# Performance work log

Measured on AMD Instinct MI355X. Metric: run time of the kernel, lower is better.

## Reference

```python
import jax, jax.numpy as jnp
import numpy as np

B, S, H, D = 1, 2048, 24, 128   # batch, img seq, heads, head_dim
RD = 64                          # rotary_emb_dim (partial RoPE)
IPS, IPD = 512, 1152             # ip tokens, ip feature dim
HID = H * D                      # 3072
EPS = 1e-6


def _heads(x):
    # (B, S, H*D) -> (B, H, S, D)
    b, s, _ = x.shape
    return x.reshape(b, s, H, D).transpose(0, 2, 1, 3)


def _rmsnorm(x, scale):
    # RMSNorm with p<0 path: rms = ||x||_2 / sqrt(D); y = scale * x / (rms + eps)
    rms = jnp.linalg.norm(x, axis=-1, keepdims=True) * (D ** -0.5)
    return scale * (x / (rms + EPS))


def _rope(x, sin, cos):
    # rotate-half RoPE on first RD channels, pass-through on the rest
    xr, xp = x[..., :RD], x[..., RD:]
    x1, x2 = jnp.split(xr, 2, axis=-1)
    rot = jnp.concatenate([-x2, x1], axis=-1)
    return jnp.concatenate([xr * cos + rot * sin, xp], axis=-1)


def setup_inputs() -> dict:
    key = jax.random.key(0)
    ks = jax.random.split(key, 16)
    std = 0.02
    inp = {
        "hidden_states": jax.random.normal(ks[0], (B, S, HID), jnp.float32),
        "ip_hidden_states": jax.random.normal(ks[1], (B, IPS, IPD), jnp.float32),
        "sin": jax.random.normal(ks[2], (S, RD), jnp.float32),
        "cos": jax.random.normal(ks[3], (S, RD), jnp.float32),
        "Wq": jax.random.normal(ks[4], (HID, HID), jnp.float32) * std,
        "bq": jnp.zeros((HID,), jnp.float32),
        "Wk": jax.random.normal(ks[5], (HID, HID), jnp.float32) * std,
        "bk": jnp.zeros((HID,), jnp.float32),
        "Wv": jax.random.normal(ks[6], (HID, HID), jnp.float32) * std,
        "bv": jnp.zeros((HID,), jnp.float32),
        "Wo": jax.random.normal(ks[7], (HID, HID), jnp.float32) * std,
        "bo": jnp.zeros((HID,), jnp.float32),
        "Wk_ip": jax.random.normal(ks[8], (HID, IPD), jnp.float32) * std,
        "bk_ip": jnp.zeros((HID,), jnp.float32),
        "Wv_ip": jax.random.normal(ks[9], (HID, IPD), jnp.float32) * std,
        "bv_ip": jnp.zeros((HID,), jnp.float32),
        "q_scale": jnp.ones((D,), jnp.float32),
        "k_scale": jnp.ones((D,), jnp.float32),
    }
    return inp


def reference(hidden_states, ip_hidden_states, sin, cos,
              Wq, bq, Wk, bk, Wv, bv, Wo, bo,
              Wk_ip, bk_ip, Wv_ip, bv_ip, q_scale, k_scale):
    scale = 1.0  # default `scale` kwarg
    # projections (self-attention: encoder_hidden_states = hidden_states)
    q = _heads(hidden_states @ Wq.T + bq)        # (B,H,S,D)
    k = _heads(hidden_states @ Wk.T + bk)
    v = _heads(hidden_states @ Wv.T + bv)
    k_ip = _heads(ip_hidden_states @ Wk_ip.T + bk_ip)   # (B,H,IPS,D)
    v_ip = _heads(ip_hidden_states @ Wv_ip.T + bv_ip)

    # IP branch uses RMS-normed, head_dim^-0.5-scaled, UNROTATED q and k_ip
    # (key_ip is rotated in the source but the rotated value is never used)
    q_norm = _rmsnorm(q, q_scale) * (D ** -0.5)
    k_ip_norm = _rmsnorm(k_ip, k_scale) * (D ** -0.5)

    # main branch: RoPE'd q/k, raw dot product (alpha=1.0, no 1/sqrt(d))
    q_rot = _rope(q, sin, cos)
    k_rot = _rope(k, sin, cos)

    scores = jnp.einsum('bhsd,bhtd->bhst', q_rot, k_rot)
    probs = jax.nn.softmax(scores, axis=-1)
    scores_ip = scale * jnp.einsum('bhsd,bhtd->bhst', q_norm, k_ip_norm)
    probs_ip = jax.nn.softmax(scores_ip, axis=-1)

    out = jnp.einsum('bhst,bhtd->bhsd', probs, v) \
        + jnp.einsum('bhst,bhtd->bhsd', probs_ip, v_ip)
    out = out.transpose(0, 2, 1, 3).reshape(B, S, HID)  # batch_to_head_dim
    out = out @ Wo.T + bo                                # to_out[0]; dropout = id
    return out
```

## Files before the change

### kernel.cpp

```cpp
#include <hip/hip_runtime.h>
#include <stdint.h>

#define S_LEN 2048
#define NH    24
#define HD    128
#define HID   3072
#define IPS   512
#define IPD   1152

using f16   = __fp16;
using f16x4 = __fp16 __attribute__((ext_vector_type(4)));
using f16x8 = __fp16 __attribute__((ext_vector_type(8)));
using f32x4 = float  __attribute__((ext_vector_type(4)));

__device__ __forceinline__ void glds16(const f16* g, f16* l) {
  __builtin_amdgcn_global_load_lds((const __attribute__((address_space(1))) void*)g,
                                   (__attribute__((address_space(3))) void*)l,
                                   16, 0, 0);
}

__global__ void k_cvt(const float* __restrict__ src, f16* __restrict__ dst, int n4) {
  int i = blockIdx.x * 256 + threadIdx.x;
  if (i >= n4) return;
  float4 v = ((const float4*)src)[i];
  f16x4 o;
  o.x = (f16)v.x; o.y = (f16)v.y; o.z = (f16)v.z; o.w = (f16)v.w;
  ((f16x4*)dst)[i] = o;
}

__global__ __launch_bounds__(256) void k_gemm_nt(
    const f16* __restrict__ A,
    const f16* __restrict__ B0, const f16* __restrict__ B1, const f16* __restrict__ B2,
    const float* __restrict__ bias0, const float* __restrict__ bias1, const float* __restrict__ bias2,
    void* __restrict__ C0, void* __restrict__ C1, void* __restrict__ C2,
    int M, int N, int K, int out_f32)
{
  const int z = blockIdx.z;
  const f16*   B    = (z == 0) ? B0 : (z == 1) ? B1 : B2;
  const float* bias = (z == 0) ? bias0 : (z == 1) ? bias1 : bias2;
  void*        Cv   = (z == 0) ? C0 : (z == 1) ? C1 : C2;

  __shared__ f16 As[128 * 32];
  __shared__ f16 Bs[128 * 32];

  const int tid  = threadIdx.x;
  const int w    = tid >> 6, l = tid & 63;
  const int quad = l >> 4,  l16 = l & 15;
  const int bm = blockIdx.y * 128, bn = blockIdx.x * 128;
  const int wm = (w >> 1) * 64,    wn = (w & 1) * 64;

  f32x4 acc[4][4] = {};

  const int r0 = w * 32;
  const f16* Ag = A + (bm + r0 + (l >> 2)) * K + (l & 3) * 8;
  const f16* Bg = B + (bn + r0 + (l >> 2)) * K + (l & 3) * 8;
  f16* lA0 = &As[r0 * 32];
  f16* lA1 = &As[(r0 + 16) * 32];
  f16* lB0 = &Bs[r0 * 32];
  f16* lB1 = &Bs[(r0 + 16) * 32];
  const int kstride16 = 16 * K;

  for (int k0 = 0; k0 < K; k0 += 32) {
    glds16(Ag + k0,             lA0);
    glds16(Ag + kstride16 + k0, lA1);
    glds16(Bg + k0,             lB0);
    glds16(Bg + kstride16 + k0, lB1);
    __syncthreads();

    f16x8 af[4], bf[4];
#pragma unroll
    for (int i = 0; i < 4; i++)
      af[i] = *(const f16x8*)&As[(wm + i * 16 + l16) * 32 + quad * 8];
#pragma unroll
    for (int j = 0; j < 4; j++)
      bf[j] = *(const f16x8*)&Bs[(wn + j * 16 + l16) * 32 + quad * 8];
#pragma unroll
    for (int i = 0; i < 4; i++)
#pragma unroll
      for (int j = 0; j < 4; j++)
        acc[i][j] = __builtin_amdgcn_mfma_f32_16x16x32_f16(af[i], bf[j], acc[i][j], 0, 0, 0);
    __syncthreads();
  }

  float bv[4];
#pragma unroll
  for (int j = 0; j < 4; j++) bv[j] = bias[bn + wn + j * 16 + l16];

#pragma unroll
  for (int i = 0; i < 4; i++) {
    const int row0 = bm + wm + i * 16 + quad * 4;
#pragma unroll
    for (int j = 0; j < 4; j++) {
      const int col = bn + wn + j * 16 + l16;
#pragma unroll
      for (int r = 0; r < 4; r++) {
        float v = acc[i][j][r] + bv[j];
        if (out_f32) ((float*)Cv)[(row0 + r) * N + col] = v;
        else         ((f16*)Cv)[(row0 + r) * N + col] = (f16)v;
      }
    }
  }
}

__global__ void k_rope(const f16* __restrict__ x, const float* __restrict__ snp,
                       const float* __restrict__ csp, f16* __restrict__ out, int total) {
  int idx = blockIdx.x * 256 + threadIdx.x;
  if (idx >= total) return;
  int s = idx / HID;
  int c = idx - s * HID;
  int d = c & (HD - 1);
  float v = (float)x[idx];
  float r;
  if (d < 64) {
    float cs = csp[s * 64 + d], sn = snp[s * 64 + d];
    if (d < 32) r = v * cs - (float)x[idx + 32] * sn;
    else        r = v * cs + (float)x[idx - 32] * sn;
  } else {
    r = v;
  }
  out[idx] = (f16)r;
}

__global__ void k_rmsnorm(const f16* __restrict__ x, const float* __restrict__ scale,
                          f16* __restrict__ out, int rows) {
  int gw = (blockIdx.x * 256 + threadIdx.x) >> 6;
  int l  = threadIdx.x & 63;
  if (gw >= rows) return;
  int base = gw * HD;
  float a = (float)x[base + 2 * l];
  float b = (float)x[base + 2 * l + 1];
  float ss = a * a + b * b;
#pragma unroll
  for (int off = 32; off >= 1; off >>= 1) ss += __shfl_xor(ss, off, 64);
  float rms = sqrtf(ss * (1.0f / HD));
  float inv = 0.08838834764831845f / (rms + 1e-6f);
  out[base + 2 * l]     = (f16)(a * scale[2 * l] * inv);
  out[base + 2 * l + 1] = (f16)(b * scale[2 * l + 1] * inv);
}

__global__ void k_kpack(const f16* __restrict__ src, f16* __restrict__ dst, int T, int nchunk) {
  int i = blockIdx.x * 256 + threadIdx.x;
  if (i >= nchunk) return;
  int d8 = i % 384;
  int t  = i / 384;
  int h  = d8 >> 4;
  int d  = (d8 & 15) * 8;
  f16x8 x = *(const f16x8*)(src + (long)i * 8);
  long off = ((((long)h * (T >> 4) + (t >> 4)) * 4 + (d >> 5)) * 64 + ((d >> 3) & 3) * 16 + (t & 15)) * 8;
  *(f16x8*)(dst + off) = x;
}

__global__ void k_krope_pack(const f16* __restrict__ src, const float* __restrict__ snp,
                             const float* __restrict__ csp, f16* __restrict__ dst,
                             int T, int nchunk) {
  int i = blockIdx.x * 256 + threadIdx.x;
  if (i >= nchunk) return;
  int d8 = i % 384;
  int t  = i / 384;
  int h  = d8 >> 4;
  int d  = (d8 & 15) * 8;
  f16x8 x = *(const f16x8*)(src + (long)i * 8);
  f16x8 o;
  if (d < 64) {
    f16x8 p = (d < 32) ? *(const f16x8*)(src + (long)i * 8 + 32)
                       : *(const f16x8*)(src + (long)i * 8 - 32);
    float sgn = (d < 32) ? -1.0f : 1.0f;
#pragma unroll
    for (int j = 0; j < 8; j++) {
      float cs = csp[t * 64 + d + j], sn = snp[t * 64 + d + j];
      o[j] = (f16)((float)x[j] * cs + sgn * (float)p[j] * sn);
    }
  } else {
    o = x;
  }
  long off = ((((long)h * (T >> 4) + (t >> 4)) * 4 + (d >> 5)) * 64 + ((d >> 3) & 3) * 16 + (t & 15)) * 8;
  *(f16x8*)(dst + off) = o;
}

__global__ __launch_bounds__(256) void k_vpack(const f16* __restrict__ v, f16* __restrict__ dst, int T) {
  __shared__ f16 Ts[128 * 72];
  int h = blockIdx.y, tb = blockIdx.x, t0 = tb * 64;
  int tid = threadIdx.x;
  int r = tid >> 2, c4 = tid & 3;
#pragma unroll
  for (int cc = 0; cc < 4; cc++) {
    int ch = c4 * 4 + cc;
    f16x8 x = *(const f16x8*)(v + (long)(t0 + r) * HID + h * HD + ch * 8);
#pragma unroll
    for (int j = 0; j < 8; j++)
      Ts[(ch * 8 + j) * 72 + r] = x[j];
  }
  __syncthreads();
  int l16 = tid & 15, jd = (tid >> 4) & 7, ks = tid >> 7;
#pragma unroll
  for (int quad = 0; quad < 4; quad++) {
    f16x8 x = *(const f16x8*)&Ts[(jd * 16 + l16) * 72 + ks * 32 + quad * 8];
    long off = ((((long)h * (T >> 6) + tb) * 2 + ks) * 8 + jd) * 512 + (quad * 16 + l16) * 8;
    *(f16x8*)(dst + off) = x;
  }
}

__global__ __launch_bounds__(256) void k_flash2(
    const f16* __restrict__ Q, const f16* __restrict__ Kp, const f16* __restrict__ Vp,
    f16* __restrict__ Opart, long part_stride, float2* __restrict__ ml, int p0,
    int T, int Tc)
{
  __shared__ f16 Ps[4][32 * 72];

  const int h    = blockIdx.y;
  const int sp   = blockIdx.z;
  const int tid  = threadIdx.x, w = tid >> 6, l = tid & 63;
  const int quad = l >> 4, l16 = l & 15;
  const int qr   = blockIdx.x * 128 + w * 32;
  const int Tt16 = T >> 4, Tt64 = T >> 6;

  f16x8 qf[2][4];
#pragma unroll
  for (int mt = 0; mt < 2; mt++)
#pragma unroll
    for (int kq = 0; kq < 4; kq++)
      qf[mt][kq] = *(const f16x8*)(Q + (long)(qr + mt * 16 + l16) * HID + h * HD + kq * 32 + quad * 8);

  f32x4 o[2][8] = {};
  float m_run[8], l_run[8];
#pragma unroll
  for (int i = 0; i < 8; i++) { m_run[i] = -1e30f; l_run[i] = 0.f; }

  f16* myP = &Ps[w][0];
  const int t_begin = sp * Tc, t_end = t_begin + Tc;

  for (int t0 = t_begin; t0 < t_end; t0 += 64) {
    f32x4 s[2][4] = {};
#pragma unroll
    for (int kq = 0; kq < 4; kq++) {
      f16x8 kf[4];
#pragma unroll
      for (int jn = 0; jn < 4; jn++)
        kf[jn] = *(const f16x8*)(Kp + (((long)(h * Tt16 + (t0 >> 4) + jn) * 4 + kq) * 64 + l) * 8);
#pragma unroll
      for (int mt = 0; mt < 2; mt++)
#pragma unroll
        for (int jn = 0; jn < 4; jn++)
          s[mt][jn] = __builtin_amdgcn_mfma_f32_16x16x32_f16(qf[mt][kq], kf[jn], s[mt][jn], 0, 0, 0);
    }

#pragma unroll
    for (int mt = 0; mt < 2; mt++) {
#pragma unroll
      for (int r = 0; r < 4; r++) {
        float mx = fmaxf(fmaxf(s[mt][0][r], s[mt][1][r]), fmaxf(s[mt][2][r], s[mt][3][r]));
        mx = fmaxf(mx, __shfl_xor(mx, 1, 64));
        mx = fmaxf(mx, __shfl_xor(mx, 2, 64));
        mx = fmaxf(mx, __shfl_xor(mx, 4, 64));
        mx = fmaxf(mx, __shfl_xor(mx, 8, 64));
        const int ri = mt * 4 + r;
        float mn = fmaxf(m_run[ri], mx);
        float al = __expf(m_run[ri] - mn);
        m_run[ri] = mn;
        float p0v = __expf(s[mt][0][r] - mn);
        float p1v = __expf(s[mt][1][r] - mn);
        float p2v = __expf(s[mt][2][r] - mn);
        float p3v = __expf(s[mt][3][r] - mn);
        s[mt][0][r] = p0v; s[mt][1][r] = p1v; s[mt][2][r] = p2v; s[mt][3][r] = p3v;
        l_run[ri] = l_run[ri] * al + (p0v + p1v + p2v + p3v);
#pragma unroll
        for (int jd = 0; jd < 8; jd++) o[mt][jd][r] *= al;
      }
    }

#pragma unroll
    for (int mt = 0; mt < 2; mt++)
#pragma unroll
      for (int jn = 0; jn < 4; jn++)
#pragma unroll
        for (int r = 0; r < 4; r++)
          myP[(mt * 16 + quad * 4 + r) * 72 + jn * 16 + l16] = (f16)s[mt][jn][r];

#pragma unroll
    for (int ks = 0; ks < 2; ks++) {
      f16x8 pf[2];
#pragma unroll
      for (int mt = 0; mt < 2; mt++)
        pf[mt] = *(const f16x8*)&myP[(mt * 16 + l16) * 72 + ks * 32 + quad * 8];
      f16x8 vf[8];
#pragma unroll
      for (int jd = 0; jd < 8; jd++)
        vf[jd] = *(const f16x8*)(Vp + ((((long)(h * Tt64 + (t0 >> 6)) * 2 + ks) * 8 + jd) * 64 + l) * 8);
#pragma unroll
      for (int jd = 0; jd < 8; jd++)
#pragma unroll
        for (int mt = 0; mt < 2; mt++)
          o[mt][jd] = __builtin_amdgcn_mfma_f32_16x16x32_f16(pf[mt], vf[jd], o[mt][jd], 0, 0, 0);
    }
  }

#pragma unroll
  for (int i = 0; i < 8; i++) {
    float v = l_run[i];
    v += __shfl_xor(v, 1, 64);
    v += __shfl_xor(v, 2, 64);
    v += __shfl_xor(v, 4, 64);
    v += __shfl_xor(v, 8, 64);
    l_run[i] = v;
  }

  f16* Od = Opart + (long)sp * part_stride;
#pragma unroll
  for (int mt = 0; mt < 2; mt++)
#pragma unroll
    for (int jd = 0; jd < 8; jd++)
#pragma unroll
      for (int r = 0; r < 4; r++) {
        int row = qr + mt * 16 + quad * 4 + r;
        int col = h * HD + jd * 16 + l16;
        Od[(long)row * HID + col] = (f16)o[mt][jd][r];
      }
  if (l16 == 0) {
#pragma unroll
    for (int mt = 0; mt < 2; mt++)
#pragma unroll
      for (int r = 0; r < 4; r++) {
        int row = qr + mt * 16 + quad * 4 + r;
        float2 v; v.x = m_run[mt * 4 + r]; v.y = l_run[mt * 4 + r];
        ml[((long)(p0 + sp) * NH + h) * S_LEN + row] = v;
      }
  }
}

__global__ void k_combine(const f16* __restrict__ O0, const f16* __restrict__ O1,
                          const f16* __restrict__ O2, const f16* __restrict__ O3,
                          const f16* __restrict__ O4, const f16* __restrict__ O5,
                          const float2* __restrict__ ml, f16* __restrict__ out, int nchunk) {
  int i = blockIdx.x * 256 + threadIdx.x;
  if (i >= nchunk) return;
  int s = i / 384, d8 = i - s * 384, h = d8 >> 4;
  long base = (long)h * S_LEN + s;
  float2 a0 = ml[0 * NH * S_LEN + base];
  float2 a1 = ml[1L * NH * S_LEN + base];
  float2 a2 = ml[2L * NH * S_LEN + base];
  float2 a3 = ml[3L * NH * S_LEN + base];
  float2 a4 = ml[4L * NH * S_LEN + base];
  float2 a5 = ml[5L * NH * S_LEN + base];
  float M1 = fmaxf(fmaxf(a0.x, a1.x), fmaxf(a2.x, a3.x));
  float e0 = __expf(a0.x - M1), e1 = __expf(a1.x - M1), e2 = __expf(a2.x - M1), e3 = __expf(a3.x - M1);
  float L1 = a0.y * e0 + a1.y * e1 + a2.y * e2 + a3.y * e3;
  float w0 = e0 / L1, w1 = e1 / L1, w2 = e2 / L1, w3 = e3 / L1;
  float M2 = fmaxf(a4.x, a5.x);
  float e4 = __expf(a4.x - M2), e5 = __expf(a5.x - M2);
  float L2 = a4.y * e4 + a5.y * e5;
  float w4 = e4 / L2, w5 = e5 / L2;
  f16x8 v0 = ((const f16x8*)O0)[i];
  f16x8 v1 = ((const f16x8*)O1)[i];
  f16x8 v2 = ((const f16x8*)O2)[i];
  f16x8 v3 = ((const f16x8*)O3)[i];
  f16x8 v4 = ((const f16x8*)O4)[i];
  f16x8 v5 = ((const f16x8*)O5)[i];
  f16x8 r;
#pragma unroll
  for (int j = 0; j < 8; j++) {
    float acc = w0 * (float)v0[j] + w1 * (float)v1[j] + w2 * (float)v2[j] + w3 * (float)v3[j]
              + w4 * (float)v4[j] + w5 * (float)v5[j];
    r[j] = (f16)acc;
  }
  ((f16x8*)out)[i] = r;
}

extern "C" void kernel_launch(void* const* d_in, const int* in_sizes, int n_in,
                              void* d_out, int out_size, void* d_ws, size_t ws_size,
                              hipStream_t stream) {
  const float* hs   = (const float*)d_in[0];
  const float* ip   = (const float*)d_in[1];
  const float* snp  = (const float*)d_in[2];
  const float* csp  = (const float*)d_in[3];
  const float* Wq   = (const float*)d_in[4];
  const float* bq   = (const float*)d_in[5];
  const float* Wk   = (const float*)d_in[6];
  const float* bk   = (const float*)d_in[7];
  const float* Wv   = (const float*)d_in[8];
  const float* bv   = (const float*)d_in[9];
  const float* Wo   = (const float*)d_in[10];
  const float* bo   = (const float*)d_in[11];
  const float* Wkip = (const float*)d_in[12];
  const float* bkip = (const float*)d_in[13];
  const float* Wvip = (const float*)d_in[14];
  const float* bvip = (const float*)d_in[15];
  const float* qs   = (const float*)d_in[16];
  const float* ks   = (const float*)d_in[17];
  float* out = (float*)d_out;

  const long n1   = 6291456;
  const long nW   = 9437184;
  const long nip  = 589824;
  const long nWip = 3538944;
  const long nk2  = 1572864;

  const long o_hs   = 0;
  const long o_Wq   = 6291456;
  const long o_Wk   = 15728640;
  const long o_Wv   = 25165824;
  const long o_Wo   = 34603008;
  const long o_ip   = 44040192;
  const long o_Wkip = 44630016;
  const long o_Wvip = 48168960;
  const long o_q    = 51707904;
  const long o_k    = 57999360;
  const long o_v    = 64290816;
  const long o_kip  = 70582272;
  const long o_vip  = 72155136;
  const long o_qrot = 73728000;
  const long o_qnorm= 80019456;
  const long o_kipn = 86310912;
  const long o_Vpip = 87883776;
  const long o_ml   = 89456640;
  const long o_Kps  = o_hs;
  const long o_Op0  = o_Wq;
  const long o_Op4  = o_Wkip;
  const long o_Op5  = o_q;
  const long o_Vps  = o_k;
  const long o_Kpip = o_kip;
  const long o_attn = o_v;

  f16* WS = (f16*)d_ws;
  auto P = [&](long off) { return WS + off; };
  float2* mlp = (float2*)(WS + o_ml);

  k_cvt<<<dim3(n1 / 1024),   256, 0, stream>>>(hs,   P(o_hs),   n1 / 4);
  k_cvt<<<dim3(nip / 1024),  256, 0, stream>>>(ip,   P(o_ip),   nip / 4);
  k_cvt<<<dim3(nW / 1024),   256, 0, stream>>>(Wq,   P(o_Wq),   nW / 4);
  k_cvt<<<dim3(nW / 1024),   256, 0, stream>>>(Wk,   P(o_Wk),   nW / 4);
  k_cvt<<<dim3(nW / 1024),   256, 0, stream>>>(Wv,   P(o_Wv),   nW / 4);
  k_cvt<<<dim3(nW / 1024),   256, 0, stream>>>(Wo,   P(o_Wo),   nW / 4);
  k_cvt<<<dim3(nWip / 1024), 256, 0, stream>>>(Wkip, P(o_Wkip), nWip / 4);
  k_cvt<<<dim3(nWip / 1024), 256, 0, stream>>>(Wvip, P(o_Wvip), nWip / 4);

  k_gemm_nt<<<dim3(24, 16, 3), 256, 0, stream>>>(P(o_hs),
      P(o_Wq), P(o_Wk), P(o_Wv), bq, bk, bv,
      P(o_q), P(o_k), P(o_v), 2048, 3072, 3072, 0);
  k_gemm_nt<<<dim3(24, 4, 2), 256, 0, stream>>>(P(o_ip),
      P(o_Wkip), P(o_Wvip), P(o_Wvip), bkip, bvip, bvip,
      P(o_kip), P(o_vip), P(o_vip), 512, 3072, 1152, 0);

  k_rope<<<dim3(n1 / 256), 256, 0, stream>>>(P(o_q), snp, csp, P(o_qrot), (int)n1);
  k_rmsnorm<<<dim3(49152 / 4), 256, 0, stream>>>(P(o_q),   qs, P(o_qnorm), 49152);
  k_krope_pack<<<dim3(786432 / 256), 256, 0, stream>>>(P(o_k), snp, csp, P(o_Kps), 2048, 786432);
  k_rmsnorm<<<dim3(12288 / 4), 256, 0, stream>>>(P(o_kip), ks, P(o_kipn), 12288);
  k_kpack<<<dim3(196608 / 256), 256, 0, stream>>>(P(o_kipn), P(o_Kpip), 512, 196608);
  k_vpack<<<dim3(32, 24), 256, 0, stream>>>(P(o_v),   P(o_Vps),  2048);
  k_vpack<<<dim3(8, 24),  256, 0, stream>>>(P(o_vip), P(o_Vpip), 512);

  k_flash2<<<dim3(16, 24, 4), 256, 0, stream>>>(P(o_qrot), P(o_Kps), P(o_Vps),
      P(o_Op0), n1, mlp, 0, 2048, 512);
  k_flash2<<<dim3(16, 24, 2), 256, 0, stream>>>(P(o_qnorm), P(o_Kpip), P(o_Vpip),
      P(o_Op4), o_Op5 - o_Op4, mlp, 4, 512, 256);

  k_combine<<<dim3(786432 / 256), 256, 0, stream>>>(
      P(o_Op0), P(o_Op0 + n1), P(o_Op0 + 2 * n1), P(o_Op0 + 3 * n1),
      P(o_Op4), P(o_Op5), mlp, P(o_attn), 786432);

  k_gemm_nt<<<dim3(24, 16, 1), 256, 0, stream>>>(P(o_attn),
      P(o_Wo), P(o_Wo), P(o_Wo), bo, bo, bo,
      out, out, out, 2048, 3072, 3072, 1);
}
```

Measured before the change: 757.0 us.

## Merge fp32 casts into one launch, swizzle GEMM LDS, fuse q and k_ip prep kernels

The eight fp32-to-fp16 cast launches become a single batched cast kernel. The GEMM's LDS tile gets an XOR swizzle on both the global-to-LDS load and the fragment reads to cut bank conflicts. Q RoPE and RMSNorm are fused into one kernel that reads q once, and the k_ip RMSNorm is fused with packing. This cuts launches and intermediate traffic, but adds a per-thread segment search in the cast kernel and more index arithmetic.

```diff
diff --git a/kernel.cpp b/kernel.cpp
--- a/kernel.cpp
+++ b/kernel.cpp
@@ -19,13 +19,17 @@
                                    16, 0, 0);
 }
 
-__global__ void k_cvt(const float* __restrict__ src, f16* __restrict__ dst, int n4) {
-  int i = blockIdx.x * 256 + threadIdx.x;
-  if (i >= n4) return;
-  float4 v = ((const float4*)src)[i];
+struct CastArgs { const float* src[8]; f16* dst[8]; long n4[8]; };
+
+__global__ void k_cvt_all(CastArgs a, long total4) {
+  long i = blockIdx.x * 256L + threadIdx.x;
+  if (i >= total4) return;
+  long r = i; int s = 0;
+  while (r >= a.n4[s]) { r -= a.n4[s]; s++; }
+  float4 v = ((const float4*)a.src[s])[r];
   f16x4 o;
   o.x = (f16)v.x; o.y = (f16)v.y; o.z = (f16)v.z; o.w = (f16)v.w;
-  ((f16x4*)dst)[i] = o;
+  ((f16x4*)a.dst[s])[r] = o;
 }
 
 __global__ __launch_bounds__(256) void k_gemm_nt(
@@ -52,13 +56,16 @@
   f32x4 acc[4][4] = {};
 
   const int r0 = w * 32;
-  const f16* Ag = A + (bm + r0 + (l >> 2)) * K + (l & 3) * 8;
-  const f16* Bg = B + (bn + r0 + (l >> 2)) * K + (l & 3) * 8;
+  const int swz_st = (l >> 3) & 3;
+  const int gchunk = ((l & 3) ^ swz_st) * 8;
+  const f16* Ag = A + (bm + r0 + (l >> 2)) * K + gchunk;
+  const f16* Bg = B + (bn + r0 + (l >> 2)) * K + gchunk;
   f16* lA0 = &As[r0 * 32];
   f16* lA1 = &As[(r0 + 16) * 32];
   f16* lB0 = &Bs[r0 * 32];
   f16* lB1 = &Bs[(r0 + 16) * 32];
   const int kstride16 = 16 * K;
+  const int swz_rd = ((l16 >> 1) & 3);
 
   for (int k0 = 0; k0 < K; k0 += 32) {
     glds16(Ag + k0,             lA0);
@@ -70,10 +77,10 @@
     f16x8 af[4], bf[4];
 #pragma unroll
     for (int i = 0; i < 4; i++)
-      af[i] = *(const f16x8*)&As[(wm + i * 16 + l16) * 32 + quad * 8];
+      af[i] = *(const f16x8*)&As[(wm + i * 16 + l16) * 32 + (quad ^ swz_rd) * 8];
 #pragma unroll
     for (int j = 0; j < 4; j++)
-      bf[j] = *(const f16x8*)&Bs[(wn + j * 16 + l16) * 32 + quad * 8];
+      bf[j] = *(const f16x8*)&Bs[(wn + j * 16 + l16) * 32 + (quad ^ swz_rd) * 8];
 #pragma unroll
     for (int i = 0; i < 4; i++)
 #pragma unroll
@@ -102,52 +109,38 @@
   }
 }
 
-__global__ void k_rope(const f16* __restrict__ x, const float* __restrict__ snp,
-                       const float* __restrict__ csp, f16* __restrict__ out, int total) {
-  int idx = blockIdx.x * 256 + threadIdx.x;
-  if (idx >= total) return;
-  int s = idx / HID;
-  int c = idx - s * HID;
-  int d = c & (HD - 1);
-  float v = (float)x[idx];
-  float r;
-  if (d < 64) {
-    float cs = csp[s * 64 + d], sn = snp[s * 64 + d];
-    if (d < 32) r = v * cs - (float)x[idx + 32] * sn;
-    else        r = v * cs + (float)x[idx - 32] * sn;
-  } else {
-    r = v;
-  }
-  out[idx] = (f16)r;
-}
-
-__global__ void k_rmsnorm(const f16* __restrict__ x, const float* __restrict__ scale,
-                          f16* __restrict__ out, int rows) {
+__global__ void k_qprep(const f16* __restrict__ x, const float* __restrict__ snp,
+                        const float* __restrict__ csp, const float* __restrict__ scale,
+                        f16* __restrict__ qrot, f16* __restrict__ qnorm, int rows) {
   int gw = (blockIdx.x * 256 + threadIdx.x) >> 6;
   int l  = threadIdx.x & 63;
   if (gw >= rows) return;
-  int base = gw * HD;
-  float a = (float)x[base + 2 * l];
-  float b = (float)x[base + 2 * l + 1];
+  long base = (long)gw * HD;
+  int s = gw / NH;
+  int d = 2 * l;
+  float a = (float)x[base + d];
+  float b = (float)x[base + d + 1];
+
   float ss = a * a + b * b;
 #pragma unroll
   for (int off = 32; off >= 1; off >>= 1) ss += __shfl_xor(ss, off, 64);
   float rms = sqrtf(ss * (1.0f / HD));
   float inv = 0.08838834764831845f / (rms + 1e-6f);
-  out[base + 2 * l]     = (f16)(a * scale[2 * l] * inv);
-  out[base + 2 * l + 1] = (f16)(b * scale[2 * l + 1] * inv);
-}
-
-__global__ void k_kpack(const f16* __restrict__ src, f16* __restrict__ dst, int T, int nchunk) {
-  int i = blockIdx.x * 256 + threadIdx.x;
-  if (i >= nchunk) return;
-  int d8 = i % 384;
-  int t  = i / 384;
-  int h  = d8 >> 4;
-  int d  = (d8 & 15) * 8;
-  f16x8 x = *(const f16x8*)(src + (long)i * 8);
-  long off = ((((long)h * (T >> 4) + (t >> 4)) * 4 + (d >> 5)) * 64 + ((d >> 3) & 3) * 16 + (t & 15)) * 8;
-  *(f16x8*)(dst + off) = x;
+  qnorm[base + d]     = (f16)(a * scale[d] * inv);
+  qnorm[base + d + 1] = (f16)(b * scale[d + 1] * inv);
+
+  float pa = __shfl_xor(a, 16, 64);
+  float pb = __shfl_xor(b, 16, 64);
+  float ra, rb;
+  if (d < 64) {
+    float sgn = (d < 32) ? -1.0f : 1.0f;
+    ra = a * csp[s * 64 + d]     + sgn * pa * snp[s * 64 + d];
+    rb = b * csp[s * 64 + d + 1] + sgn * pb * snp[s * 64 + d + 1];
+  } else {
+    ra = a; rb = b;
+  }
+  qrot[base + d]     = (f16)ra;
+  qrot[base + d + 1] = (f16)rb;
 }
 
 __global__ void k_krope_pack(const f16* __restrict__ src, const float* __restrict__ snp,
@@ -173,6 +166,32 @@
   } else {
     o = x;
   }
+  long off = ((((long)h * (T >> 4) + (t >> 4)) * 4 + (d >> 5)) * 64 + ((d >> 3) & 3) * 16 + (t & 15)) * 8;
+  *(f16x8*)(dst + off) = o;
+}
+
+__global__ void k_rms_pack(const f16* __restrict__ x, const float* __restrict__ scale,
+                           f16* __restrict__ dst, int T, int rows) {
+  int gw  = (blockIdx.x * 256 + threadIdx.x) >> 6;
+  int l   = threadIdx.x & 63;
+  int sub = l >> 4, l16 = l & 15;
+  int row = gw * 4 + sub;
+  if (row >= rows) return;
+  int t = row / NH, h = row - t * NH;
+  int d = l16 * 8;
+  f16x8 v = *(const f16x8*)(x + (long)row * HD + d);
+  float ss = 0.f;
+#pragma unroll
+  for (int j = 0; j < 8; j++) { float f = (float)v[j]; ss += f * f; }
+  ss += __shfl_xor(ss, 1, 64);
+  ss += __shfl_xor(ss, 2, 64);
+  ss += __shfl_xor(ss, 4, 64);
+  ss += __shfl_xor(ss, 8, 64);
+  float rms = sqrtf(ss * (1.0f / HD));
+  float inv = 0.08838834764831845f / (rms + 1e-6f);
+  f16x8 o;
+#pragma unroll
+  for (int j = 0; j < 8; j++) o[j] = (f16)((float)v[j] * scale[d + j] * inv);
   long off = ((((long)h * (T >> 4) + (t >> 4)) * 4 + (d >> 5)) * 64 + ((d >> 3) & 3) * 16 + (t & 15)) * 8;
   *(f16x8*)(dst + off) = o;
 }
@@ -392,7 +411,6 @@
   const long nW   = 9437184;
   const long nip  = 589824;
   const long nWip = 3538944;
-  const long nk2  = 1572864;
 
   const long o_hs   = 0;
   const long o_Wq   = 6291456;
@@ -424,14 +442,17 @@
   auto P = [&](long off) { return WS + off; };
   float2* mlp = (float2*)(WS + o_ml);
 
-  k_cvt<<<dim3(n1 / 1024),   256, 0, stream>>>(hs,   P(o_hs),   n1 / 4);
-  k_cvt<<<dim3(nip / 1024),  256, 0, stream>>>(ip,   P(o_ip),   nip / 4);
-  k_cvt<<<dim3(nW / 1024),   256, 0, stream>>>(Wq,   P(o_Wq),   nW / 4);
-  k_cvt<<<dim3(nW / 1024),   256, 0, stream>>>(Wk,   P(o_Wk),   nW / 4);
-  k_cvt<<<dim3(nW / 1024),   256, 0, stream>>>(Wv,   P(o_Wv),   nW / 4);
-  k_cvt<<<dim3(nW / 1024),   256, 0, stream>>>(Wo,   P(o_Wo),   nW / 4);
-  k_cvt<<<dim3(nWip / 1024), 256, 0, stream>>>(Wkip, P(o_Wkip), nWip / 4);
-  k_cvt<<<dim3(nWip / 1024), 256, 0, stream>>>(Wvip, P(o_Wvip), nWip / 4);
+  CastArgs ca;
+  ca.src[0] = hs;   ca.dst[0] = P(o_hs);   ca.n4[0] = n1 / 4;
+  ca.src[1] = ip;   ca.dst[1] = P(o_ip);   ca.n4[1] = nip / 4;
+  ca.src[2] = Wq;   ca.dst[2] = P(o_Wq);   ca.n4[2] = nW / 4;
+  ca.src[3] = Wk;   ca.dst[3] = P(o_Wk);   ca.n4[3] = nW / 4;
+  ca.src[4] = Wv;   ca.dst[4] = P(o_Wv);   ca.n4[4] = nW / 4;
+  ca.src[5] = Wo;   ca.dst[5] = P(o_Wo);   ca.n4[5] = nW / 4;
+  ca.src[6] = Wkip; ca.dst[6] = P(o_Wkip); ca.n4[6] = nWip / 4;
+  ca.src[7] = Wvip; ca.dst[7] = P(o_Wvip); ca.n4[7] = nWip / 4;
+  const long total4 = (n1 + nip + 4 * nW + 2 * nWip) / 4;
+  k_cvt_all<<<dim3((total4 + 255) / 256), 256, 0, stream>>>(ca, total4);
 
   k_gemm_nt<<<dim3(24, 16, 3), 256, 0, stream>>>(P(o_hs),
       P(o_Wq), P(o_Wk), P(o_Wv), bq, bk, bv,
@@ -440,11 +461,9 @@
       P(o_Wkip), P(o_Wvip), P(o_Wvip), bkip, bvip, bvip,
       P(o_kip), P(o_vip), P(o_vip), 512, 3072, 1152, 0);
 
-  k_rope<<<dim3(n1 / 256), 256, 0, stream>>>(P(o_q), snp, csp, P(o_qrot), (int)n1);
-  k_rmsnorm<<<dim3(49152 / 4), 256, 0, stream>>>(P(o_q),   qs, P(o_qnorm), 49152);
+  k_qprep<<<dim3(49152 / 4), 256, 0, stream>>>(P(o_q), snp, csp, qs, P(o_qrot), P(o_qnorm), 49152);
   k_krope_pack<<<dim3(786432 / 256), 256, 0, stream>>>(P(o_k), snp, csp, P(o_Kps), 2048, 786432);
-  k_rmsnorm<<<dim3(12288 / 4), 256, 0, stream>>>(P(o_kip), ks, P(o_kipn), 12288);
-  k_kpack<<<dim3(196608 / 256), 256, 0, stream>>>(P(o_kipn), P(o_Kpip), 512, 196608);
+  k_rms_pack<<<dim3(12288 / 16), 256, 0, stream>>>(P(o_kip), ks, P(o_Kpip), 512, 12288);
   k_vpack<<<dim3(32, 24), 256, 0, stream>>>(P(o_v),   P(o_Vps),  2048);
   k_vpack<<<dim3(8, 24),  256, 0, stream>>>(P(o_vip), P(o_Vpip), 512);
 
```

Measured after the change: 732.6 us. -3.2%, faster.
